# Optimization experiments

Measured on AMD Instinct MI355X. Metric: run time of the kernel, lower is better.

Reference implementation:

```python
import jax, jax.numpy as jnp
import numpy as np

D_MODEL = 1024
N_HEADS = 16
D_K = D_MODEL // N_HEADS
MAX_REL = 128
SEQ = 1024
BATCH = 4


def setup_inputs() -> dict:
    key = jax.random.key(0)
    ks = jax.random.split(key, 8)
    x = jax.random.normal(ks[0], (SEQ, BATCH, D_MODEL), dtype=jnp.float32)
    # nn.Linear weights: shape (out, in), applied as x @ W.T
    w_q = jax.random.normal(ks[1], (D_MODEL, D_MODEL), dtype=jnp.float32) * (1.0 / np.sqrt(D_MODEL))
    w_k = jax.random.normal(ks[2], (D_MODEL, D_MODEL), dtype=jnp.float32) * (1.0 / np.sqrt(D_MODEL))
    w_v = jax.random.normal(ks[3], (D_MODEL, D_MODEL), dtype=jnp.float32) * (1.0 / np.sqrt(D_MODEL))
    w_o = jax.random.normal(ks[4], (D_MODEL, D_MODEL), dtype=jnp.float32) * (1.0 / np.sqrt(D_MODEL))
    b_o = jnp.zeros((D_MODEL,), dtype=jnp.float32)
    rel_k = jax.random.normal(ks[5], (2 * MAX_REL + 1, D_K), dtype=jnp.float32)
    rel_v = jax.random.normal(ks[6], (2 * MAX_REL + 1, D_K), dtype=jnp.float32)
    return {"x": x, "w_q": w_q, "w_k": w_k, "w_v": w_v, "w_o": w_o, "b_o": b_o,
            "rel_k": rel_k, "rel_v": rel_v}


def _relative_positions(seq_len: int) -> jnp.ndarray:
    pos = jnp.arange(seq_len)
    rel = pos[:, None] - pos[None, :]
    rel = jnp.clip(rel, -MAX_REL, MAX_REL) + MAX_REL
    return rel  # [s, t] int indices into relative tables


def reference(x, w_q, w_k, w_v, w_o, b_o, rel_k, rel_v):
    seq_len, batch, _ = x.shape
    scale = 1.0 / np.sqrt(D_K)
    Q = (x @ w_q.T).reshape(seq_len, batch, N_HEADS, D_K)
    K = (x @ w_k.T).reshape(seq_len, batch, N_HEADS, D_K)
    V = (x @ w_v.T).reshape(seq_len, batch, N_HEADS, D_K)

    rel_idx = _relative_positions(seq_len)          # [s, t]
    rk = rel_k[rel_idx]                              # [s, t, d_k]
    rv = rel_v[rel_idx]                              # [s, t, d_k]

    scores = jnp.einsum('sbhd,tbhd->sbth', Q, K) * scale
    scores = scores + jnp.einsum('sbhd,std->sbth', Q, rk) * scale
    # NOTE: original torch code softmaxes over dim=-1 of [s,b,t,h], i.e. the
    # head axis; reproduced faithfully here.
    attn = jax.nn.softmax(scores, axis=-1)           # [s, b, t, h]

    out = jnp.einsum('sbth,tbhd->sbhd', attn, V)
    out = out + jnp.einsum('sbth,std->sbhd', attn, rv)
    out = out.reshape(seq_len, batch, D_MODEL)
    return out @ w_o.T + b_o
```

## Files before the change

### kernel.cpp

```cpp
#include <hip/hip_runtime.h>
#include <stdint.h>

#define DI __device__ __forceinline__

typedef __attribute__((ext_vector_type(8))) short bfx8;
typedef __attribute__((ext_vector_type(4))) short bfx4;
typedef __attribute__((ext_vector_type(4))) float f4;

DI unsigned short f2bf(float x){
  unsigned u = __float_as_uint(x);
  u = (u + 0x7FFFu + ((u >> 16) & 1u)) >> 16;
  return (unsigned short)u;
}
DI float bf2f(unsigned short h){ return __uint_as_float(((unsigned)h) << 16); }

DI f4 mfma32(bfx8 a, bfx8 b, f4 c){
  return __builtin_amdgcn_mfma_f32_16x16x32_bf16(a, b, c, 0, 0, 0);
}
#if __has_builtin(__builtin_amdgcn_mfma_f32_16x16x16bf16_1k)
DI f4 mfma16(bfx4 a, bfx4 b, f4 c){
  return __builtin_amdgcn_mfma_f32_16x16x16bf16_1k(a, b, c, 0, 0, 0);
}
#else
DI f4 mfma16(bfx4 a, bfx4 b, f4 c){
  f4 d = c;
  asm volatile("v_mfma_f32_16x16x16_bf16 %0, %1, %2, %0" : "+v"(d) : "v"(a), "v"(b));
  return d;
}
#endif

DI void gload16(const void* g, void* l){
  __builtin_amdgcn_global_load_lds(
      (__attribute__((address_space(1))) void*)g,
      (__attribute__((address_space(3))) void*)l, 16, 0, 0);
}


__global__ void k_cast(const float* __restrict__ src, unsigned short* __restrict__ dst, int n4){
  int i = blockIdx.x*256 + threadIdx.x;
  if (i < n4){
    const float4 v = ((const float4*)src)[i];
    bfx4 o;
    o[0] = (short)f2bf(v.x); o[1] = (short)f2bf(v.y);
    o[2] = (short)f2bf(v.z); o[3] = (short)f2bf(v.w);
    *(bfx4*)(dst + (size_t)i*4) = o;
  }
}

__global__ void k_castw(const float* __restrict__ s0, const float* __restrict__ s1,
                        const float* __restrict__ s2, const float* __restrict__ s3,
                        unsigned short* __restrict__ dst){
  int i = blockIdx.x*256 + threadIdx.x;
  const float* src = (blockIdx.y==0) ? s0 : (blockIdx.y==1) ? s1 : (blockIdx.y==2) ? s2 : s3;
  const float4 v = ((const float4*)src)[i];
  bfx4 o;
  o[0] = (short)f2bf(v.x); o[1] = (short)f2bf(v.y);
  o[2] = (short)f2bf(v.z); o[3] = (short)f2bf(v.w);
  *(bfx4*)(dst + (size_t)blockIdx.y*1048576 + (size_t)i*4) = o;
}

__global__ void k_relprep(const float* __restrict__ rlk, const float* __restrict__ rlv,
                          unsigned short* __restrict__ relk_bf, unsigned short* __restrict__ relvT_bf){
  int i = blockIdx.x*256 + threadIdx.x;
  if (i < 272*64){
    int r = i >> 6, d = i & 63;
    relk_bf[i] = (r < 257) ? f2bf(rlk[r*64 + d]) : (unsigned short)0;
  }
  if (i < 64*288){
    int d = i / 288, r = i % 288;
    relvT_bf[i] = (r < 257) ? f2bf(rlv[(size_t)r*64 + d]) : (unsigned short)0;
  }
}

__global__ __launch_bounds__(256, 3) void k_qkv(
    const unsigned short* __restrict__ xbf, const unsigned short* __restrict__ wqkv,
    unsigned short* __restrict__ Qf, unsigned short* __restrict__ Kf,
    unsigned short* __restrict__ Vf)
{
  __shared__ __align__(16) unsigned short smem[2][8192];
  const int nt = blockIdx.x;
  const int b  = blockIdx.y;
  const int st = blockIdx.z;
  const int w = threadIdx.x >> 6, lane = threadIdx.x & 63;
  const int wr = w >> 1, wc = w & 1;
  const int p = lane & 15, g = lane >> 4;
  const int s0 = st*128;
  const int n0 = nt*128;
  const f4 fz = {0.f,0.f,0.f,0.f};
  f4 acc[4][4];
#pragma unroll
  for (int m=0;m<4;++m)
#pragma unroll
    for (int n=0;n<4;++n) acc[m][n] = fz;

  const int j0 = w*2, j1 = w*2 + 1;
  const unsigned short* gA = xbf  + (size_t)((s0 + p)*4 + b)*1024 + g*8;
  const unsigned short* gB = wqkv + (size_t)(n0 + p)*1024 + g*8;

  {
    unsigned short* d0 = &smem[0][0];
    gload16(gA + (size_t)j0*65536, d0 + j0*512);
    gload16(gA + (size_t)j1*65536, d0 + j1*512);
    gload16(gB + (size_t)j0*16384, d0 + 4096 + j0*512);
    gload16(gB + (size_t)j1*16384, d0 + 4096 + j1*512);
  }

  for (int it=0; it<32; ++it){
    const int cur = it & 1;
    if (it < 31){
      const int kn = (it+1)*32;
      unsigned short* dn = &smem[cur^1][0];
      gload16(gA + (size_t)j0*65536 + kn, dn + j0*512);
      gload16(gA + (size_t)j1*65536 + kn, dn + j1*512);
      gload16(gB + (size_t)j0*16384 + kn, dn + 4096 + j0*512);
      gload16(gB + (size_t)j1*16384 + kn, dn + 4096 + j1*512);
      asm volatile("s_waitcnt vmcnt(4)" ::: "memory");
    } else {
      asm volatile("s_waitcnt vmcnt(0)" ::: "memory");
    }
    __builtin_amdgcn_sched_barrier(0);
    __builtin_amdgcn_s_barrier();
    __builtin_amdgcn_sched_barrier(0);
    {
      const unsigned short* Ab = &smem[cur][0];
      bfx8 af[4], bfr[4];
#pragma unroll
      for (int m=0;m<4;++m) af[m] = *(const bfx8*)(Ab + (wr*4+m)*512 + lane*8);
#pragma unroll
      for (int n=0;n<4;++n) bfr[n] = *(const bfx8*)(Ab + 4096 + (wc*4+n)*512 + lane*8);
#pragma unroll
      for (int m=0;m<4;++m)
#pragma unroll
        for (int n=0;n<4;++n)
          acc[m][n] = mfma32(af[m], bfr[n], acc[m][n]);
    }
    __builtin_amdgcn_sched_barrier(0);
    __builtin_amdgcn_s_barrier();
    __builtin_amdgcn_sched_barrier(0);
  }

  const int n64 = n0 + wc*64;
  const int sec = n64 >> 10;
  const int h = (n64 & 1023) >> 6;
  float* es = (float*)&smem[0][0] + w*1280;

  if (sec < 2){
    const float scl = (sec == 0) ? 0.125f : 1.0f;
    unsigned short* dst = (sec == 0) ? Qf : Kf;
#pragma unroll
    for (int m=0;m<4;++m){
#pragma unroll
      for (int n=0;n<4;++n)
#pragma unroll
        for (int r=0;r<4;++r)
          es[(4*g + r)*80 + 16*n + p] = acc[m][n][r] * scl;
      __syncthreads();
      f4 v0 = *(const f4*)&es[p*80 + 8*g];
      f4 v1 = *(const f4*)&es[p*80 + 8*g + 4];
      f4 v2 = *(const f4*)&es[p*80 + 32 + 8*g];
      f4 v3 = *(const f4*)&es[p*80 + 32 + 8*g + 4];
      bfx8 lo, hi;
#pragma unroll
      for (int j=0;j<4;++j){
        lo[j]   = (short)f2bf(v0[j]);
        lo[j+4] = (short)f2bf(v1[j]);
        hi[j]   = (short)f2bf(v2[j]);
        hi[j+4] = (short)f2bf(v3[j]);
      }
      size_t fb = ((size_t)(b*16 + h)*64 + (st*8 + wr*4 + m))*1024 + (size_t)lane*16;
      *(bfx8*)(dst + fb) = lo;
      *(bfx8*)(dst + fb + 8) = hi;
      __syncthreads();
    }
  } else {
#pragma unroll
    for (int m=0;m<4;++m){
#pragma unroll
      for (int n=0;n<4;++n)
        *(f4*)&es[(16*n + p)*20 + 4*g] = acc[m][n];
      __syncthreads();
      f4 vv0 = *(const f4*)&es[(p)*20 + 4*g];
      f4 vv1 = *(const f4*)&es[(16 + p)*20 + 4*g];
      f4 vv2 = *(const f4*)&es[(32 + p)*20 + 4*g];
      f4 vv3 = *(const f4*)&es[(48 + p)*20 + 4*g];
      bfx8 lo, hi;
#pragma unroll
      for (int j=0;j<4;++j){
        lo[j]   = (short)f2bf(vv0[j]);
        lo[j+4] = (short)f2bf(vv1[j]);
        hi[j]   = (short)f2bf(vv2[j]);
        hi[j+4] = (short)f2bf(vv3[j]);
      }
      size_t fb = ((size_t)(b*16 + h)*64 + (st*8 + wr*4 + m))*1024 + (size_t)lane*16;
      *(bfx8*)(Vf + fb) = lo;
      *(bfx8*)(Vf + fb + 8) = hi;
      __syncthreads();
    }
  }
}

__global__ __launch_bounds__(256) void k_qr(
    const unsigned short* __restrict__ Qf, const unsigned short* __restrict__ relk,
    unsigned short* __restrict__ Qr2)
{
  __shared__ __align__(16) unsigned short sst[16][16][24];
  const int bx = blockIdx.x;
  const int b  = bx & 3;
  const int st = (bx >> 2) & 63;
  const int uh = bx >> 8;
  const int w = threadIdx.x >> 6, lane = threadIdx.x & 63;
  const int p = lane & 15, g = lane >> 4;
  const int s0 = st << 4;
  const f4 fz = {0.f,0.f,0.f,0.f};

  bfx8 a0[4], a1[4];
#pragma unroll
  for (int hh=0; hh<4; ++hh){
    size_t fb = (((size_t)(b*16 + w*4 + hh))*64 + st)*1024 + (size_t)lane*16;
    a0[hh] = *(const bfx8*)(Qf + fb);
    a1[hh] = *(const bfx8*)(Qf + fb + 8);
  }

  const int c0 = uh ? 9 : 0;
  const int c1 = uh ? 17 : 9;
  const int so = threadIdx.x >> 4, uo = threadIdx.x & 15;

  for (int c=c0; c<c1; ++c){
    const int r0 = c << 4;
    bfx8 b0 = *(const bfx8*)(relk + (size_t)(r0 + p)*64 + 8*g);
    bfx8 b1 = *(const bfx8*)(relk + (size_t)(r0 + p)*64 + 32 + 8*g);
#pragma unroll
    for (int hh=0; hh<4; ++hh){
      f4 acc = mfma32(a1[hh], b1, mfma32(a0[hh], b0, fz));
#pragma unroll
      for (int r=0; r<4; ++r)
        sst[4*g + r][p][w*4 + hh] = f2bf(acc[r]);
    }
    __syncthreads();
    bfx8 v0 = *(const bfx8*)&sst[so][uo][0];
    bfx8 v1 = *(const bfx8*)&sst[so][uo][8];
    size_t ga = (((size_t)b*1024 + s0 + so)*272 + r0 + uo)*16;
    *(bfx8*)(Qr2 + ga) = v0;
    *(bfx8*)(Qr2 + ga + 8) = v1;
    __syncthreads();
  }
}

__global__ __launch_bounds__(256, 2) void k_s(
    const unsigned short* __restrict__ Qf, const unsigned short* __restrict__ Kf,
    const unsigned short* __restrict__ Qr2, float* __restrict__ ivf)
{
  const int pbid = blockIdx.x;
  const int b   = pbid & 3;
  const int ttg = (pbid >> 2) & 15;
  const int st  = pbid >> 6;
  const int w = threadIdx.x >> 6, lane = threadIdx.x & 63;
  const int tt = ttg*4 + w;
  const int p = lane & 15, g = lane >> 4;
  const int s0 = st << 4, t0 = tt << 4;
  const int s = s0 + p;
  const f4 fz = {0.f,0.f,0.f,0.f};

  bfx8 rv[4][2];
#pragma unroll
  for (int r=0; r<4; ++r){
    int t = t0 + 4*g + r;
    int u = s - t + 128; u = u < 0 ? 0 : (u > 256 ? 256 : u);
    const unsigned short* q = Qr2 + (((size_t)b*1024 + s)*272 + u)*16;
    rv[r][0] = *(const bfx8*)q;
    rv[r][1] = *(const bfx8*)(q + 8);
  }

  const unsigned short* qbp = Qf + ((size_t)(b*16)*64 + st)*1024 + (size_t)lane*16;
  const unsigned short* kbp = Kf + ((size_t)(b*16)*64 + tt)*1024 + (size_t)lane*16;

  bfx8 qq[16][2], kk[16][2];
#define LOADH(H) { \
    qq[H][0] = *(const bfx8*)(qbp + (size_t)(H)*65536); \
    qq[H][1] = *(const bfx8*)(qbp + (size_t)(H)*65536 + 8); \
    kk[H][0] = *(const bfx8*)(kbp + (size_t)(H)*65536); \
    kk[H][1] = *(const bfx8*)(kbp + (size_t)(H)*65536 + 8); }

  LOADH(0) LOADH(1) LOADH(2) LOADH(3)

  f4 ps = fz;
#pragma unroll
  for (int h=0; h<16; ++h){
    if (h + 4 < 16){
      const int hn = h + 4;
      qq[hn][0] = *(const bfx8*)(qbp + (size_t)hn*65536);
      qq[hn][1] = *(const bfx8*)(qbp + (size_t)hn*65536 + 8);
      kk[hn][0] = *(const bfx8*)(kbp + (size_t)hn*65536);
      kk[hn][1] = *(const bfx8*)(kbp + (size_t)hn*65536 + 8);
    }
    f4 sc = mfma32(kk[h][1], qq[h][1], mfma32(kk[h][0], qq[h][0], fz));
    const int hg = h >> 3, hr = h & 7;
#pragma unroll
    for (int r=0; r<4; ++r)
      ps[r] += __expf(sc[r] + bf2f((unsigned short)rv[r][hg][hr]));
  }
#undef LOADH

  f4 inv;
#pragma unroll
  for (int r=0; r<4; ++r) inv[r] = 1.0f / ps[r];
  *(f4*)(ivf + (((size_t)(b*64 + tt)*64 + st)*64 + lane)*4) = inv;
}

__global__ __launch_bounds__(256, 3) void k_far(
    const unsigned short* __restrict__ Qf, const unsigned short* __restrict__ Kf,
    const unsigned short* __restrict__ Vf, const unsigned short* __restrict__ Qr2,
    const float* __restrict__ ivf, float* __restrict__ tails,
    unsigned short* __restrict__ op)
{
  __shared__ __align__(16) float slab[4][16][68];
  const int pbid  = blockIdx.x;
  const int b     = pbid & 3;
  const int part  = (pbid >> 2) & 3;
  const int hhalf = (pbid >> 4) & 1;
  const int st    = pbid >> 5;
  const int s0 = st << 4;
  const int w = threadIdx.x >> 6, lane = threadIdx.x & 63;
  const int p = lane & 15, g = lane >> 4;
  const int s = s0 + p;
  const int h0 = hhalf*8 + w*2;
  const f4 fz = {0.f,0.f,0.f,0.f};

  bfx8 qf[2][2]; float qr0[2], qr1[2];
#pragma unroll
  for (int hh=0; hh<2; ++hh){
    size_t bh = (size_t)(b*16 + h0 + hh);
    size_t qb = (bh*64 + st)*1024 + (size_t)lane*16;
    qf[hh][0] = *(const bfx8*)(Qf + qb);
    qf[hh][1] = *(const bfx8*)(Qf + qb + 8);
    qr0[hh] = bf2f(Qr2[(((size_t)b*1024 + s)*272 + 0)*16 + (h0+hh)]);
    qr1[hh] = bf2f(Qr2[(((size_t)b*1024 + s)*272 + 256)*16 + (h0+hh)]);
  }

  f4 o[2][4];
#pragma unroll
  for (int hh=0; hh<2; ++hh)
#pragma unroll
    for (int df=0; df<4; ++df) o[hh][df] = fz;
  float tl0[2] = {0.f,0.f};
  float tl1[2] = {0.f,0.f};

  const int tlo = (st-8 < 0) ? 0 : st-8;
  const int thi = (st+8 > 63) ? 63 : st+8;
  const int nband = thi - tlo + 1;
  const int nfar = 64 - nband;

  bfx8 kc[2][2]; bfx4 vc[2][4]; f4 is;
  bfx8 kn[2][2]; bfx4 vn[2][4]; f4 isn;

  int idx = part;
  {
    const int ti = (idx < tlo) ? idx : idx + nband;
#pragma unroll
    for (int hh=0; hh<2; ++hh){
      size_t fb = (((size_t)(b*16 + h0 + hh))*64 + ti)*1024 + (size_t)lane*16;
      kc[hh][0] = *(const bfx8*)(Kf + fb);
      kc[hh][1] = *(const bfx8*)(Kf + fb + 8);
#pragma unroll
      for (int df=0; df<4; ++df)
        vc[hh][df] = *(const bfx4*)(Vf + fb + df*4);
    }
    is = *(const f4*)(ivf + (((size_t)(b*64 + ti)*64 + st)*64 + lane)*4);
  }

  while (idx < nfar){
    const int idn = idx + 4;
    if (idn < nfar){
      const int tn = (idn < tlo) ? idn : idn + nband;
#pragma unroll
      for (int hh=0; hh<2; ++hh){
        size_t fb = (((size_t)(b*16 + h0 + hh))*64 + tn)*1024 + (size_t)lane*16;
        kn[hh][0] = *(const bfx8*)(Kf + fb);
        kn[hh][1] = *(const bfx8*)(Kf + fb + 8);
#pragma unroll
        for (int df=0; df<4; ++df)
          vn[hh][df] = *(const bfx4*)(Vf + fb + df*4);
      }
      isn = *(const f4*)(ivf + (((size_t)(b*64 + tn)*64 + st)*64 + lane)*4);
    }

    const int ti = (idx < tlo) ? idx : idx + nband;
    const bool hiSide = (ti < st);
#pragma unroll
    for (int hh=0; hh<2; ++hh){
      f4 sc = mfma32(kc[hh][1], qf[hh][1], mfma32(kc[hh][0], qf[hh][0], fz));
      const float qa = hiSide ? qr1[hh] : qr0[hh];
      f4 at;
#pragma unroll
      for (int r=0; r<4; ++r) at[r] = __expf(sc[r] + qa) * is[r];
      float tsum = at[0] + at[1] + at[2] + at[3];
      if (hiSide) tl1[hh] += tsum; else tl0[hh] += tsum;
      bfx4 pk;
#pragma unroll
      for (int r=0; r<4; ++r) pk[r] = (short)f2bf(at[r]);
#pragma unroll
      for (int df=0; df<4; ++df)
        o[hh][df] = mfma16(vc[hh][df], pk, o[hh][df]);
    }

    if (idn < nfar){
#pragma unroll
      for (int hh=0; hh<2; ++hh){
        kc[hh][0] = kn[hh][0]; kc[hh][1] = kn[hh][1];
#pragma unroll
        for (int df=0; df<4; ++df) vc[hh][df] = vn[hh][df];
      }
      is = isn;
    }
    idx = idn;
  }

#pragma unroll
  for (int hh=0; hh<2; ++hh){
    float v0 = tl0[hh];
    v0 += __shfl_xor(v0, 16, 64);
    v0 += __shfl_xor(v0, 32, 64);
    float v1 = tl1[hh];
    v1 += __shfl_xor(v1, 16, 64);
    v1 += __shfl_xor(v1, 32, 64);
    if (g == 0){
      size_t tix = ((size_t)(part*64 + b*16 + h0 + hh)*1024 + s)*2;
      tails[tix + 0] = v0;
      tails[tix + 1] = v1;
    }
  }

  unsigned short* dst = op + (size_t)part * 4194304;
#pragma unroll
  for (int hh=0; hh<2; ++hh){
    float (*tb)[68] = slab[w];
#pragma unroll
    for (int df=0; df<4; ++df)
      *(f4*)&tb[p][df*16 + 4*g] = o[hh][df];
    __syncthreads();
    const int srow = lane >> 2, quad = lane & 3;
    f4 r0 = *(const f4*)&tb[srow][quad*16 + 0];
    f4 r1 = *(const f4*)&tb[srow][quad*16 + 4];
    f4 r2 = *(const f4*)&tb[srow][quad*16 + 8];
    f4 r3 = *(const f4*)&tb[srow][quad*16 + 12];
    bfx8 pa, pb;
#pragma unroll
    for (int j=0; j<4; ++j){
      pa[j]   = (short)f2bf(r0[j]);
      pa[j+4] = (short)f2bf(r1[j]);
      pb[j]   = (short)f2bf(r2[j]);
      pb[j+4] = (short)f2bf(r3[j]);
    }
    size_t addr = ((size_t)b*1024 + s0 + srow)*1024 + (h0+hh)*64 + quad*16;
    *(bfx8*)(dst + addr) = pa;
    *(bfx8*)(dst + addr + 8) = pb;
    __syncthreads();
  }
}

__global__ __launch_bounds__(256, 2) void k_near(
    const unsigned short* __restrict__ Qf, const unsigned short* __restrict__ Kf,
    const unsigned short* __restrict__ Vf, const unsigned short* __restrict__ Qr2,
    const float* __restrict__ ivf, const unsigned short* __restrict__ relvT,
    const float* __restrict__ relv, const float* __restrict__ tails,
    const unsigned short* __restrict__ op, unsigned short* __restrict__ out1)
{
  __shared__ __align__(16) unsigned short skew[128*264];
  const int pbid = blockIdx.x;
  const int xcd = pbid & 7;
  const int b = xcd >> 1;
  const int hhalf = (pbid >> 3) & 1;
  const int st = ((pbid >> 4) << 1) | (xcd & 1);
  const int s0 = st << 4;
  const int w = threadIdx.x >> 6;
  const int lane = threadIdx.x & 63;
  const int p = lane & 15, g = lane >> 4;
  const int s = s0 + p;
  const int hl0 = w * 2;
  const int h0 = hhalf*8 + hl0;
  const f4 fz = {0.f,0.f,0.f,0.f};

  {
    unsigned* zp = (unsigned*)skew + w*4224;
    for (int i = lane; i < 4224; i += 64) zp[i] = 0u;
  }

  bfx8 qf[2][2];
#pragma unroll
  for (int hh=0; hh<2; ++hh){
    size_t qb = (((size_t)(b*16 + h0 + hh))*64 + st)*1024 + (size_t)lane*16;
    qf[hh][0] = *(const bfx8*)(Qf + qb);
    qf[hh][1] = *(const bfx8*)(Qf + qb + 8);
  }

  f4 o[2][4];
#pragma unroll
  for (int hh=0; hh<2; ++hh)
#pragma unroll
    for (int df=0; df<4; ++df) o[hh][df] = fz;

  float tl0[2] = {0.f,0.f};
  float tl1[2] = {0.f,0.f};

  const int tlo = (st-8 < 0) ? 0 : st-8;
  const int thi = (st+8 > 63) ? 63 : st+8;

  bfx8 kc[2][2]; bfx4 vc[2][4]; unsigned short qc[2][4]; f4 is;
  bfx8 kn[2][2]; bfx4 vn[2][4]; unsigned short qn[2][4]; f4 isn;

#pragma unroll
  for (int hh=0; hh<2; ++hh){
    size_t bh = (size_t)(b*16 + h0 + hh);
    size_t fb = (bh*64 + tlo)*1024 + (size_t)lane*16;
    kc[hh][0] = *(const bfx8*)(Kf + fb);
    kc[hh][1] = *(const bfx8*)(Kf + fb + 8);
#pragma unroll
    for (int df=0; df<4; ++df)
      vc[hh][df] = *(const bfx4*)(Vf + fb + df*4);
#pragma unroll
    for (int r=0; r<4; ++r){
      int t = (tlo<<4) + 4*g + r;
      int u = s - t + 128; u = u < 0 ? 0 : (u > 256 ? 256 : u);
      qc[hh][r] = Qr2[(((size_t)b*1024 + s)*272 + u)*16 + (h0+hh)];
    }
  }
  is = *(const f4*)(ivf + (((size_t)(b*64 + tlo)*64 + st)*64 + lane)*4);

  for (int ti = tlo; ti <= thi; ++ti){
    const int t0 = ti << 4;

    if (ti < thi){
      const int tn = ti + 1;
#pragma unroll
      for (int hh=0; hh<2; ++hh){
        size_t bh = (size_t)(b*16 + h0 + hh);
        size_t fb = (bh*64 + tn)*1024 + (size_t)lane*16;
        kn[hh][0] = *(const bfx8*)(Kf + fb);
        kn[hh][1] = *(const bfx8*)(Kf + fb + 8);
#pragma unroll
        for (int df=0; df<4; ++df)
          vn[hh][df] = *(const bfx4*)(Vf + fb + df*4);
#pragma unroll
        for (int r=0; r<4; ++r){
          int t = (tn<<4) + 4*g + r;
          int u = s - t + 128; u = u < 0 ? 0 : (u > 256 ? 256 : u);
          qn[hh][r] = Qr2[(((size_t)b*1024 + s)*272 + u)*16 + (h0+hh)];
        }
      }
      isn = *(const f4*)(ivf + (((size_t)(b*64 + tn)*64 + st)*64 + lane)*4);
    }

#pragma unroll
    for (int hh=0; hh<2; ++hh){
      f4 sc = mfma32(kc[hh][1], qf[hh][1], mfma32(kc[hh][0], qf[hh][0], fz));
      f4 at;
#pragma unroll
      for (int r=0; r<4; ++r) at[r] = __expf(sc[r] + bf2f(qc[hh][r])) * is[r];
      const int row = (hl0 + hh)*16 + p;
#pragma unroll
      for (int r=0; r<4; ++r){
        int t = t0 + 4*g + r;
        int u = s - t + 128;
        float a = at[r];
        if (u <= 0) tl0[hh] += a;
        else if (u >= 256) tl1[hh] += a;
        else skew[row*264 + u] = f2bf(a);
      }
      bfx4 pk;
#pragma unroll
      for (int r=0; r<4; ++r) pk[r] = (short)f2bf(at[r]);
#pragma unroll
      for (int df=0; df<4; ++df)
        o[hh][df] = mfma16(vc[hh][df], pk, o[hh][df]);
    }

    if (ti < thi){
#pragma unroll
      for (int hh=0; hh<2; ++hh){
#pragma unroll
        for (int kf=0; kf<2; ++kf) kc[hh][kf] = kn[hh][kf];
#pragma unroll
        for (int df=0; df<4; ++df) vc[hh][df] = vn[hh][df];
#pragma unroll
        for (int r=0; r<4; ++r) qc[hh][r] = qn[hh][r];
      }
      is = isn;
    }
  }

  __syncthreads();

  f4 acc2[2][4];
#pragma unroll
  for (int hh=0; hh<2; ++hh)
#pragma unroll
    for (int df=0; df<4; ++df) acc2[hh][df] = fz;
#pragma unroll
  for (int k0=0; k0<256; k0+=32){
    bfx8 bb0 = *(const bfx8*)&skew[(hl0*16 + p)*264 + k0 + 8*g];
    bfx8 bb1 = *(const bfx8*)&skew[((hl0+1)*16 + p)*264 + k0 + 8*g];
#pragma unroll
    for (int df=0; df<4; ++df){
      bfx8 a = *(const bfx8*)(relvT + (size_t)(df*16 + p)*288 + k0 + 8*g);
      acc2[0][df] = mfma32(a, bb0, acc2[0][df]);
      acc2[1][df] = mfma32(a, bb1, acc2[1][df]);
    }
  }

  f4 rv0[4], rv1[4];
#pragma unroll
  for (int df=0; df<4; ++df){
    rv0[df] = *(const f4*)(relv + df*16 + 4*g);
    rv1[df] = *(const f4*)(relv + 16384 + df*16 + 4*g);
  }
#pragma unroll
  for (int hh=0; hh<2; ++hh){
    float tv0 = tl0[hh];
    tv0 += __shfl_xor(tv0, 16, 64);
    tv0 += __shfl_xor(tv0, 32, 64);
    float tv1 = tl1[hh];
    tv1 += __shfl_xor(tv1, 16, 64);
    tv1 += __shfl_xor(tv1, 32, 64);
    size_t bh = (size_t)(b*16 + h0 + hh);
#pragma unroll
    for (int part=0; part<4; ++part){
      size_t tix = ((size_t)(part*64) + bh)*2048 + (size_t)s*2;
      tv0 += tails[tix + 0];
      tv1 += tails[tix + 1];
    }
#pragma unroll
    for (int df=0; df<4; ++df)
#pragma unroll
      for (int r=0; r<4; ++r)
        o[hh][df][r] += acc2[hh][df][r] + tv0*rv0[df][r] + tv1*rv1[df][r];
  }

  __syncthreads();

  float* slabBase = (float*)skew;
  float (*tb)[68] = (float(*)[68])(slabBase + w*(16*68));
#pragma unroll
  for (int hh=0; hh<2; ++hh){
#pragma unroll
    for (int df=0; df<4; ++df)
      *(f4*)&tb[p][df*16 + 4*g] = o[hh][df];
    __syncthreads();
    const int srow = lane >> 2, quad = lane & 3;
    f4 r0 = *(const f4*)&tb[srow][quad*16 + 0];
    f4 r1 = *(const f4*)&tb[srow][quad*16 + 4];
    f4 r2 = *(const f4*)&tb[srow][quad*16 + 8];
    f4 r3 = *(const f4*)&tb[srow][quad*16 + 12];
    size_t addr = ((size_t)b*1024 + s0 + srow)*1024 + (h0+hh)*64 + quad*16;
    bfx8 pa, pb;
#pragma unroll
    for (int j=0; j<4; ++j){
      float a0 = r0[j], a1 = r1[j], a2 = r2[j], a3 = r3[j];
#pragma unroll
      for (int part=0; part<4; ++part){
        const unsigned short* pp = op + (size_t)part*4194304 + addr;
        bfx8 q0 = *(const bfx8*)pp;
        bfx8 q1 = *(const bfx8*)(pp + 8);
        a0 += bf2f((unsigned short)q0[j]);
        a1 += bf2f((unsigned short)q0[j+4]);
        a2 += bf2f((unsigned short)q1[j]);
        a3 += bf2f((unsigned short)q1[j+4]);
      }
      pa[j]   = (short)f2bf(a0);
      pa[j+4] = (short)f2bf(a1);
      pb[j]   = (short)f2bf(a2);
      pb[j+4] = (short)f2bf(a3);
    }
    *(bfx8*)(out1 + addr) = pa;
    *(bfx8*)(out1 + addr + 8) = pb;
    __syncthreads();
  }
}

__global__ __launch_bounds__(256) void k_wo(
    const unsigned short* __restrict__ out1, const unsigned short* __restrict__ wo,
    const float* __restrict__ bo, float* __restrict__ dout)
{
  __shared__ __align__(16) unsigned short smem[2][6144];
  const int nt = blockIdx.x;
  const int mt = blockIdx.y;
  const int w = threadIdx.x >> 6, lane = threadIdx.x & 63;
  const int wr = w >> 1, wc = w & 1;
  const int p = lane & 15, g = lane >> 4;
  const int m0 = mt*64, n0 = nt*128;
  const f4 fz = {0.f,0.f,0.f,0.f};
  f4 acc[2][4];
#pragma unroll
  for (int m=0;m<2;++m)
#pragma unroll
    for (int n=0;n<4;++n) acc[m][n] = fz;

  const int j0 = w*2, j1 = w*2 + 1;
  const unsigned short* gA = out1 + (size_t)(m0 + p)*1024 + g*8;
  const unsigned short* gB = wo   + (size_t)(n0 + p)*1024 + g*8;

  {
    unsigned short* d0 = &smem[0][0];
    gload16(gA + (size_t)w*16384, d0 + w*512);
    gload16(gB + (size_t)j0*16384, d0 + 2048 + j0*512);
    gload16(gB + (size_t)j1*16384, d0 + 2048 + j1*512);
  }

  for (int it=0; it<32; ++it){
    const int cur = it & 1;
    if (it < 31){
      const int kn = (it+1)*32;
      unsigned short* dn = &smem[cur^1][0];
      gload16(gA + (size_t)w*16384 + kn, dn + w*512);
      gload16(gB + (size_t)j0*16384 + kn, dn + 2048 + j0*512);
      gload16(gB + (size_t)j1*16384 + kn, dn + 2048 + j1*512);
      asm volatile("s_waitcnt vmcnt(3)" ::: "memory");
    } else {
      asm volatile("s_waitcnt vmcnt(0)" ::: "memory");
    }
    __builtin_amdgcn_sched_barrier(0);
    __builtin_amdgcn_s_barrier();
    __builtin_amdgcn_sched_barrier(0);
    {
      const unsigned short* Ab = &smem[cur][0];
      bfx8 af[2], bfr[4];
#pragma unroll
      for (int m=0;m<2;++m) af[m] = *(const bfx8*)(Ab + (wr*2+m)*512 + lane*8);
#pragma unroll
      for (int n=0;n<4;++n) bfr[n] = *(const bfx8*)(Ab + 2048 + (wc*4+n)*512 + lane*8);
#pragma unroll
      for (int m=0;m<2;++m)
#pragma unroll
        for (int n=0;n<4;++n)
          acc[m][n] = mfma32(af[m], bfr[n], acc[m][n]);
    }
    __builtin_amdgcn_sched_barrier(0);
    __builtin_amdgcn_s_barrier();
    __builtin_amdgcn_sched_barrier(0);
  }

#pragma unroll
  for (int n=0;n<4;++n){
    const int col = n0 + wc*64 + n*16 + p;
    const float bias = bo[col];
#pragma unroll
    for (int m=0;m<2;++m)
#pragma unroll
      for (int r=0;r<4;++r){
        int row = m0 + wr*32 + m*16 + 4*g + r;
        int bb = row >> 10, s = row & 1023;
        dout[((size_t)s*4 + bb)*1024 + col] = acc[m][n][r] + bias;
      }
  }
}

extern "C" void kernel_launch(void* const* d_in, const int* in_sizes, int n_in,
                              void* d_out, int out_size, void* d_ws, size_t ws_size,
                              hipStream_t stream){
  const float* x   = (const float*)d_in[0];
  const float* wq  = (const float*)d_in[1];
  const float* wk  = (const float*)d_in[2];
  const float* wv  = (const float*)d_in[3];
  const float* wo  = (const float*)d_in[4];
  const float* bo  = (const float*)d_in[5];
  const float* rlk = (const float*)d_in[6];
  const float* rlv = (const float*)d_in[7];
  char* ws = (char*)d_ws;

  unsigned short* x_bf    = (unsigned short*)(ws + 0);
  unsigned short* wq_bf   = (unsigned short*)(ws + 8388608);
  unsigned short* relk_bf = (unsigned short*)(ws + 16777216);
  unsigned short* relvT_bf= (unsigned short*)(ws + 16812032);
  unsigned short* Qf      = (unsigned short*)(ws + 16848896);
  unsigned short* Kf      = (unsigned short*)(ws + 25237504);
  unsigned short* Vf      = (unsigned short*)(ws + 33626112);
  unsigned short* Qr2     = (unsigned short*)(ws + 42014720);
  float*          tails   = (float*)        (ws + 77666304);
  unsigned short* op      = (unsigned short*)(ws + 79763456);
  unsigned short* out1    = (unsigned short*)(ws + 113317888);
  float*          ivf     = (float*)        (ws + 121706496);
  unsigned short* wo_bf   = (unsigned short*)(ws + 14680064);

  k_cast<<<4096, 256, 0, stream>>>(x, x_bf, 1048576);
  k_castw<<<dim3(1024,4), 256, 0, stream>>>(wq, wk, wv, wo, wq_bf);
  k_relprep<<<72, 256, 0, stream>>>(rlk, rlv, relk_bf, relvT_bf);

  k_qkv<<<dim3(24,4,8), 256, 0, stream>>>(x_bf, wq_bf, Qf, Kf, Vf);
  k_qr<<<512, 256, 0, stream>>>(Qf, relk_bf, Qr2);

  k_s  <<<4096, 256, 0, stream>>>(Qf, Kf, Qr2, ivf);
  k_far<<<2048, 256, 0, stream>>>(Qf, Kf, Vf, Qr2, ivf, tails, op);
  k_near<<<512, 256, 0, stream>>>(Qf, Kf, Vf, Qr2, ivf, relvT_bf, rlv, tails, op, out1);
  k_wo<<<dim3(8,64), 256, 0, stream>>>(out1, wo_bf, bo, (float*)d_out);
}
```

Before: 248.9 us.

## Merge far-band and near-band attention kernels into one pass

Removes k_far and folds its far-key work into k_near (renamed k_attn), so each block now loops over all 64 key tiles and branches per tile between the near-band skew path and the far constant-bias path. This drops the partial-output buffer, the tails buffer, a kernel launch, and the four-way reduction reads in the epilogue. The cost is less parallelism: the far work previously ran on 2048 blocks at occupancy 3 and now runs serially inside 512 blocks at occupancy 2, which lengthens each block's loop.

```diff
diff --git a/kernel.cpp b/kernel.cpp
--- a/kernel.cpp
+++ b/kernel.cpp
@@ -307,163 +307,11 @@
   *(f4*)(ivf + (((size_t)(b*64 + tt)*64 + st)*64 + lane)*4) = inv;
 }
 
-__global__ __launch_bounds__(256, 3) void k_far(
-    const unsigned short* __restrict__ Qf, const unsigned short* __restrict__ Kf,
-    const unsigned short* __restrict__ Vf, const unsigned short* __restrict__ Qr2,
-    const float* __restrict__ ivf, float* __restrict__ tails,
-    unsigned short* __restrict__ op)
-{
-  __shared__ __align__(16) float slab[4][16][68];
-  const int pbid  = blockIdx.x;
-  const int b     = pbid & 3;
-  const int part  = (pbid >> 2) & 3;
-  const int hhalf = (pbid >> 4) & 1;
-  const int st    = pbid >> 5;
-  const int s0 = st << 4;
-  const int w = threadIdx.x >> 6, lane = threadIdx.x & 63;
-  const int p = lane & 15, g = lane >> 4;
-  const int s = s0 + p;
-  const int h0 = hhalf*8 + w*2;
-  const f4 fz = {0.f,0.f,0.f,0.f};
-
-  bfx8 qf[2][2]; float qr0[2], qr1[2];
-#pragma unroll
-  for (int hh=0; hh<2; ++hh){
-    size_t bh = (size_t)(b*16 + h0 + hh);
-    size_t qb = (bh*64 + st)*1024 + (size_t)lane*16;
-    qf[hh][0] = *(const bfx8*)(Qf + qb);
-    qf[hh][1] = *(const bfx8*)(Qf + qb + 8);
-    qr0[hh] = bf2f(Qr2[(((size_t)b*1024 + s)*272 + 0)*16 + (h0+hh)]);
-    qr1[hh] = bf2f(Qr2[(((size_t)b*1024 + s)*272 + 256)*16 + (h0+hh)]);
-  }
-
-  f4 o[2][4];
-#pragma unroll
-  for (int hh=0; hh<2; ++hh)
-#pragma unroll
-    for (int df=0; df<4; ++df) o[hh][df] = fz;
-  float tl0[2] = {0.f,0.f};
-  float tl1[2] = {0.f,0.f};
-
-  const int tlo = (st-8 < 0) ? 0 : st-8;
-  const int thi = (st+8 > 63) ? 63 : st+8;
-  const int nband = thi - tlo + 1;
-  const int nfar = 64 - nband;
-
-  bfx8 kc[2][2]; bfx4 vc[2][4]; f4 is;
-  bfx8 kn[2][2]; bfx4 vn[2][4]; f4 isn;
-
-  int idx = part;
-  {
-    const int ti = (idx < tlo) ? idx : idx + nband;
-#pragma unroll
-    for (int hh=0; hh<2; ++hh){
-      size_t fb = (((size_t)(b*16 + h0 + hh))*64 + ti)*1024 + (size_t)lane*16;
-      kc[hh][0] = *(const bfx8*)(Kf + fb);
-      kc[hh][1] = *(const bfx8*)(Kf + fb + 8);
-#pragma unroll
-      for (int df=0; df<4; ++df)
-        vc[hh][df] = *(const bfx4*)(Vf + fb + df*4);
-    }
-    is = *(const f4*)(ivf + (((size_t)(b*64 + ti)*64 + st)*64 + lane)*4);
-  }
-
-  while (idx < nfar){
-    const int idn = idx + 4;
-    if (idn < nfar){
-      const int tn = (idn < tlo) ? idn : idn + nband;
-#pragma unroll
-      for (int hh=0; hh<2; ++hh){
-        size_t fb = (((size_t)(b*16 + h0 + hh))*64 + tn)*1024 + (size_t)lane*16;
-        kn[hh][0] = *(const bfx8*)(Kf + fb);
-        kn[hh][1] = *(const bfx8*)(Kf + fb + 8);
-#pragma unroll
-        for (int df=0; df<4; ++df)
-          vn[hh][df] = *(const bfx4*)(Vf + fb + df*4);
-      }
-      isn = *(const f4*)(ivf + (((size_t)(b*64 + tn)*64 + st)*64 + lane)*4);
-    }
-
-    const int ti = (idx < tlo) ? idx : idx + nband;
-    const bool hiSide = (ti < st);
-#pragma unroll
-    for (int hh=0; hh<2; ++hh){
-      f4 sc = mfma32(kc[hh][1], qf[hh][1], mfma32(kc[hh][0], qf[hh][0], fz));
-      const float qa = hiSide ? qr1[hh] : qr0[hh];
-      f4 at;
-#pragma unroll
-      for (int r=0; r<4; ++r) at[r] = __expf(sc[r] + qa) * is[r];
-      float tsum = at[0] + at[1] + at[2] + at[3];
-      if (hiSide) tl1[hh] += tsum; else tl0[hh] += tsum;
-      bfx4 pk;
-#pragma unroll
-      for (int r=0; r<4; ++r) pk[r] = (short)f2bf(at[r]);
-#pragma unroll
-      for (int df=0; df<4; ++df)
-        o[hh][df] = mfma16(vc[hh][df], pk, o[hh][df]);
-    }
-
-    if (idn < nfar){
-#pragma unroll
-      for (int hh=0; hh<2; ++hh){
-        kc[hh][0] = kn[hh][0]; kc[hh][1] = kn[hh][1];
-#pragma unroll
-        for (int df=0; df<4; ++df) vc[hh][df] = vn[hh][df];
-      }
-      is = isn;
-    }
-    idx = idn;
-  }
-
-#pragma unroll
-  for (int hh=0; hh<2; ++hh){
-    float v0 = tl0[hh];
-    v0 += __shfl_xor(v0, 16, 64);
-    v0 += __shfl_xor(v0, 32, 64);
-    float v1 = tl1[hh];
-    v1 += __shfl_xor(v1, 16, 64);
-    v1 += __shfl_xor(v1, 32, 64);
-    if (g == 0){
-      size_t tix = ((size_t)(part*64 + b*16 + h0 + hh)*1024 + s)*2;
-      tails[tix + 0] = v0;
-      tails[tix + 1] = v1;
-    }
-  }
-
-  unsigned short* dst = op + (size_t)part * 4194304;
-#pragma unroll
-  for (int hh=0; hh<2; ++hh){
-    float (*tb)[68] = slab[w];
-#pragma unroll
-    for (int df=0; df<4; ++df)
-      *(f4*)&tb[p][df*16 + 4*g] = o[hh][df];
-    __syncthreads();
-    const int srow = lane >> 2, quad = lane & 3;
-    f4 r0 = *(const f4*)&tb[srow][quad*16 + 0];
-    f4 r1 = *(const f4*)&tb[srow][quad*16 + 4];
-    f4 r2 = *(const f4*)&tb[srow][quad*16 + 8];
-    f4 r3 = *(const f4*)&tb[srow][quad*16 + 12];
-    bfx8 pa, pb;
-#pragma unroll
-    for (int j=0; j<4; ++j){
-      pa[j]   = (short)f2bf(r0[j]);
-      pa[j+4] = (short)f2bf(r1[j]);
-      pb[j]   = (short)f2bf(r2[j]);
-      pb[j+4] = (short)f2bf(r3[j]);
-    }
-    size_t addr = ((size_t)b*1024 + s0 + srow)*1024 + (h0+hh)*64 + quad*16;
-    *(bfx8*)(dst + addr) = pa;
-    *(bfx8*)(dst + addr + 8) = pb;
-    __syncthreads();
-  }
-}
-
-__global__ __launch_bounds__(256, 2) void k_near(
+__global__ __launch_bounds__(256, 2) void k_attn(
     const unsigned short* __restrict__ Qf, const unsigned short* __restrict__ Kf,
     const unsigned short* __restrict__ Vf, const unsigned short* __restrict__ Qr2,
     const float* __restrict__ ivf, const unsigned short* __restrict__ relvT,
-    const float* __restrict__ relv, const float* __restrict__ tails,
-    const unsigned short* __restrict__ op, unsigned short* __restrict__ out1)
+    const float* __restrict__ relv, unsigned short* __restrict__ out1)
 {
   __shared__ __align__(16) unsigned short skew[128*264];
   const int pbid = blockIdx.x;
@@ -485,12 +333,14 @@
     for (int i = lane; i < 4224; i += 64) zp[i] = 0u;
   }
 
-  bfx8 qf[2][2];
+  bfx8 qf[2][2]; float qr0[2], qr1[2];
 #pragma unroll
   for (int hh=0; hh<2; ++hh){
     size_t qb = (((size_t)(b*16 + h0 + hh))*64 + st)*1024 + (size_t)lane*16;
     qf[hh][0] = *(const bfx8*)(Qf + qb);
     qf[hh][1] = *(const bfx8*)(Qf + qb + 8);
+    qr0[hh] = bf2f(Qr2[(((size_t)b*1024 + s)*272 + 0)*16 + (h0+hh)]);
+    qr1[hh] = bf2f(Qr2[(((size_t)b*1024 + s)*272 + 256)*16 + (h0+hh)]);
   }
 
   f4 o[2][4];
@@ -511,25 +361,30 @@
 #pragma unroll
   for (int hh=0; hh<2; ++hh){
     size_t bh = (size_t)(b*16 + h0 + hh);
-    size_t fb = (bh*64 + tlo)*1024 + (size_t)lane*16;
+    size_t fb = (bh*64 + 0)*1024 + (size_t)lane*16;
     kc[hh][0] = *(const bfx8*)(Kf + fb);
     kc[hh][1] = *(const bfx8*)(Kf + fb + 8);
 #pragma unroll
     for (int df=0; df<4; ++df)
       vc[hh][df] = *(const bfx4*)(Vf + fb + df*4);
-#pragma unroll
-    for (int r=0; r<4; ++r){
-      int t = (tlo<<4) + 4*g + r;
-      int u = s - t + 128; u = u < 0 ? 0 : (u > 256 ? 256 : u);
-      qc[hh][r] = Qr2[(((size_t)b*1024 + s)*272 + u)*16 + (h0+hh)];
-    }
-  }
-  is = *(const f4*)(ivf + (((size_t)(b*64 + tlo)*64 + st)*64 + lane)*4);
-
-  for (int ti = tlo; ti <= thi; ++ti){
+  }
+  if (0 >= tlo){
+#pragma unroll
+    for (int hh=0; hh<2; ++hh)
+#pragma unroll
+      for (int r=0; r<4; ++r){
+        int t = 4*g + r;
+        int u = s - t + 128; u = u < 0 ? 0 : (u > 256 ? 256 : u);
+        qc[hh][r] = Qr2[(((size_t)b*1024 + s)*272 + u)*16 + (h0+hh)];
+      }
+  }
+  is = *(const f4*)(ivf + (((size_t)(b*64 + 0)*64 + st)*64 + lane)*4);
+
+  for (int ti = 0; ti < 64; ++ti){
     const int t0 = ti << 4;
-
-    if (ti < thi){
+    const bool nearT = (ti >= tlo) && (ti <= thi);
+
+    if (ti < 63){
       const int tn = ti + 1;
 #pragma unroll
       for (int hh=0; hh<2; ++hh){
@@ -540,41 +395,65 @@
 #pragma unroll
         for (int df=0; df<4; ++df)
           vn[hh][df] = *(const bfx4*)(Vf + fb + df*4);
+      }
+      if (tn >= tlo && tn <= thi){
+#pragma unroll
+        for (int hh=0; hh<2; ++hh)
+#pragma unroll
+          for (int r=0; r<4; ++r){
+            int t = (tn<<4) + 4*g + r;
+            int u = s - t + 128; u = u < 0 ? 0 : (u > 256 ? 256 : u);
+            qn[hh][r] = Qr2[(((size_t)b*1024 + s)*272 + u)*16 + (h0+hh)];
+          }
+      }
+      isn = *(const f4*)(ivf + (((size_t)(b*64 + tn)*64 + st)*64 + lane)*4);
+    }
+
+    if (nearT){
+#pragma unroll
+      for (int hh=0; hh<2; ++hh){
+        f4 sc = mfma32(kc[hh][1], qf[hh][1], mfma32(kc[hh][0], qf[hh][0], fz));
+        f4 at;
+#pragma unroll
+        for (int r=0; r<4; ++r) at[r] = __expf(sc[r] + bf2f(qc[hh][r])) * is[r];
+        const int row = (hl0 + hh)*16 + p;
 #pragma unroll
         for (int r=0; r<4; ++r){
-          int t = (tn<<4) + 4*g + r;
-          int u = s - t + 128; u = u < 0 ? 0 : (u > 256 ? 256 : u);
-          qn[hh][r] = Qr2[(((size_t)b*1024 + s)*272 + u)*16 + (h0+hh)];
+          int t = t0 + 4*g + r;
+          int u = s - t + 128;
+          float a = at[r];
+          if (u <= 0) tl0[hh] += a;
+          else if (u >= 256) tl1[hh] += a;
+          else skew[row*264 + u] = f2bf(a);
         }
-      }
-      isn = *(const f4*)(ivf + (((size_t)(b*64 + tn)*64 + st)*64 + lane)*4);
-    }
-
-#pragma unroll
-    for (int hh=0; hh<2; ++hh){
-      f4 sc = mfma32(kc[hh][1], qf[hh][1], mfma32(kc[hh][0], qf[hh][0], fz));
-      f4 at;
-#pragma unroll
-      for (int r=0; r<4; ++r) at[r] = __expf(sc[r] + bf2f(qc[hh][r])) * is[r];
-      const int row = (hl0 + hh)*16 + p;
-#pragma unroll
-      for (int r=0; r<4; ++r){
-        int t = t0 + 4*g + r;
-        int u = s - t + 128;
-        float a = at[r];
-        if (u <= 0) tl0[hh] += a;
-        else if (u >= 256) tl1[hh] += a;
-        else skew[row*264 + u] = f2bf(a);
-      }
-      bfx4 pk;
-#pragma unroll
-      for (int r=0; r<4; ++r) pk[r] = (short)f2bf(at[r]);
-#pragma unroll
-      for (int df=0; df<4; ++df)
-        o[hh][df] = mfma16(vc[hh][df], pk, o[hh][df]);
-    }
-
-    if (ti < thi){
+        bfx4 pk;
+#pragma unroll
+        for (int r=0; r<4; ++r) pk[r] = (short)f2bf(at[r]);
+#pragma unroll
+        for (int df=0; df<4; ++df)
+          o[hh][df] = mfma16(vc[hh][df], pk, o[hh][df]);
+      }
+    } else {
+      const bool hiSide = (ti < st);
+#pragma unroll
+      for (int hh=0; hh<2; ++hh){
+        f4 sc = mfma32(kc[hh][1], qf[hh][1], mfma32(kc[hh][0], qf[hh][0], fz));
+        const float qa = hiSide ? qr1[hh] : qr0[hh];
+        f4 at;
+#pragma unroll
+        for (int r=0; r<4; ++r) at[r] = __expf(sc[r] + qa) * is[r];
+        float tsum = at[0] + at[1] + at[2] + at[3];
+        if (hiSide) tl1[hh] += tsum; else tl0[hh] += tsum;
+        bfx4 pk;
+#pragma unroll
+        for (int r=0; r<4; ++r) pk[r] = (short)f2bf(at[r]);
+#pragma unroll
+        for (int df=0; df<4; ++df)
+          o[hh][df] = mfma16(vc[hh][df], pk, o[hh][df]);
+      }
+    }
+
+    if (ti < 63){
 #pragma unroll
       for (int hh=0; hh<2; ++hh){
 #pragma unroll
@@ -621,13 +500,6 @@
     float tv1 = tl1[hh];
     tv1 += __shfl_xor(tv1, 16, 64);
     tv1 += __shfl_xor(tv1, 32, 64);
-    size_t bh = (size_t)(b*16 + h0 + hh);
-#pragma unroll
-    for (int part=0; part<4; ++part){
-      size_t tix = ((size_t)(part*64) + bh)*2048 + (size_t)s*2;
-      tv0 += tails[tix + 0];
-      tv1 += tails[tix + 1];
-    }
 #pragma unroll
     for (int df=0; df<4; ++df)
 #pragma unroll
@@ -654,21 +526,10 @@
     bfx8 pa, pb;
 #pragma unroll
     for (int j=0; j<4; ++j){
-      float a0 = r0[j], a1 = r1[j], a2 = r2[j], a3 = r3[j];
-#pragma unroll
-      for (int part=0; part<4; ++part){
-        const unsigned short* pp = op + (size_t)part*4194304 + addr;
-        bfx8 q0 = *(const bfx8*)pp;
-        bfx8 q1 = *(const bfx8*)(pp + 8);
-        a0 += bf2f((unsigned short)q0[j]);
-        a1 += bf2f((unsigned short)q0[j+4]);
-        a2 += bf2f((unsigned short)q1[j]);
-        a3 += bf2f((unsigned short)q1[j+4]);
-      }
-      pa[j]   = (short)f2bf(a0);
-      pa[j+4] = (short)f2bf(a1);
-      pb[j]   = (short)f2bf(a2);
-      pb[j+4] = (short)f2bf(a3);
+      pa[j]   = (short)f2bf(r0[j]);
+      pa[j+4] = (short)f2bf(r1[j]);
+      pb[j]   = (short)f2bf(r2[j]);
+      pb[j+4] = (short)f2bf(r3[j]);
     }
     *(bfx8*)(out1 + addr) = pa;
     *(bfx8*)(out1 + addr + 8) = pb;
@@ -774,8 +635,6 @@
   unsigned short* Kf      = (unsigned short*)(ws + 25237504);
   unsigned short* Vf      = (unsigned short*)(ws + 33626112);
   unsigned short* Qr2     = (unsigned short*)(ws + 42014720);
-  float*          tails   = (float*)        (ws + 77666304);
-  unsigned short* op      = (unsigned short*)(ws + 79763456);
   unsigned short* out1    = (unsigned short*)(ws + 113317888);
   float*          ivf     = (float*)        (ws + 121706496);
   unsigned short* wo_bf   = (unsigned short*)(ws + 14680064);
@@ -787,8 +646,7 @@
   k_qkv<<<dim3(24,4,8), 256, 0, stream>>>(x_bf, wq_bf, Qf, Kf, Vf);
   k_qr<<<512, 256, 0, stream>>>(Qf, relk_bf, Qr2);
 
-  k_s  <<<4096, 256, 0, stream>>>(Qf, Kf, Qr2, ivf);
-  k_far<<<2048, 256, 0, stream>>>(Qf, Kf, Vf, Qr2, ivf, tails, op);
-  k_near<<<512, 256, 0, stream>>>(Qf, Kf, Vf, Qr2, ivf, relvT_bf, rlv, tails, op, out1);
+  k_s   <<<4096, 256, 0, stream>>>(Qf, Kf, Qr2, ivf);
+  k_attn<<<512, 256, 0, stream>>>(Qf, Kf, Vf, Qr2, ivf, relvT_bf, rlv, out1);
   k_wo<<<dim3(8,64), 256, 0, stream>>>(out1, wo_bf, bo, (float*)d_out);
 }
```

Measured after the change: 226.6 us. 9.0% less time.
